# Optimization experiments

Hardware: AMD Instinct MI355X
Metric: run time of the kernel (lower is better)

The kernel has to match this reference:

```python
import jax, jax.numpy as jnp
import numpy as np


def setup_inputs() -> dict:
    key = jax.random.key(0)
    ks = jax.random.split(key, 12)
    C, H, L, P = 256, 8, 4, 4
    Lq, Lx = 2048, 300
    iss = jnp.array([[64, 64], [32, 32], [16, 16], [8, 8]], dtype=jnp.int32)
    Len_in = int(np.sum(np.array(iss)[:, 0] * np.array(iss)[:, 1]))  # 5440
    lsi = jnp.array([0, 4096, 5120, 5376], dtype=jnp.int32)
    return {
        "query": jax.random.normal(ks[0], (1, Lq, C), jnp.float32),
        "reference_points": jax.random.uniform(ks[1], (1, Lq, L, 2), jnp.float32),
        "input_flatten": jax.random.normal(ks[2], (1, Len_in, C), jnp.float32),
        "input_spatial_shapes": iss,
        "add_keys": jax.random.normal(ks[3], (1, Lx, C), jnp.float32),
        "input_level_start_index": lsi,
        "W_off": jax.random.normal(ks[4], (H * L * P * 2, C), jnp.float32) * 0.01,
        "b_off": jax.random.normal(ks[5], (H * L * P * 2,), jnp.float32),
        "W_attn": jax.random.normal(ks[6], (H * (L + 1), C, C), jnp.float32) * 0.05,
        "W_v": jax.random.normal(ks[7], (H * 2, C, C), jnp.float32) * 0.05,
        "b_v": jax.random.normal(ks[8], (H * 2, C), jnp.float32) * 0.01,
        "W_mix": jax.random.normal(ks[9], (C, H + 1), jnp.float32) * 0.5,
    }


def reference(query, reference_points, input_flatten, input_spatial_shapes,
              add_keys, input_level_start_index, W_off, b_off, W_attn, W_v, b_v, W_mix):
    N, Lq, C = query.shape
    L = input_spatial_shapes.shape[0]
    H = W_v.shape[0] // 2
    P = W_off.shape[0] // (H * L * 2)

    # sampling locations: ref (x,y in [0,1]) + offsets / (W,H)
    off = (query @ W_off.T + b_off).reshape(N, Lq, H, L, P, 2)
    wh = input_spatial_shapes[:, ::-1].astype(query.dtype)  # (L,2) = (W,H)
    loc = reference_points[:, :, None, :, None, :] + off / wh[None, None, None, :, None, :]

    # get_keys: truncating index computation + gather (faithful to original)
    loc = jnp.clip(loc, 0.0, 0.999)
    iss_f = input_spatial_shapes.astype(loc.dtype)[None, None, None, :, None, :]
    idx = (loc * iss_f).astype(jnp.int32)  # (N,Lq,H,L,P,2): (int(x*H_l), int(y*W_l))
    lin = (idx[..., 0]
           + idx[..., 1] * input_spatial_shapes[:, 0].astype(jnp.int32)[None, None, None, :, None]
           + input_level_start_index.astype(jnp.int32)[None, None, None, :, None])
    keys = input_flatten[0][lin[0]]                # (Lq,H,L,P,C)
    keys = jnp.transpose(keys, (1, 2, 3, 0, 4))    # (H,L,P,Lq,C)

    head_w = jax.nn.softmax(W_mix.T, axis=0)       # (H+1,C)
    qf = query[0]                                  # (Lq,C)
    ak = add_keys[0]                               # (Lx,C)

    # per-head, per-level similarity (replicates original overlapping index h*L+lvl)
    Ws = W_attn[jnp.arange(H)[:, None] * L + jnp.arange(L)[None, :]]  # (H,L,C,C)
    T = jnp.einsum('hlce,hlpqe->hlcpq', Ws, keys)  # (H,L,C,P,Lq)
    # faithful reshape quirk: (C, P*Lq) viewed as (P, Lq, C)
    T = T.reshape(H, L, P, Lq, C)
    attn_s = jnp.einsum('hlpqc,qc->hlpq', T, qf).reshape(H, L * P, Lq)

    Wadd = W_attn[jnp.arange(H) * L + L]           # (H,C,C)
    attn_a = jnp.einsum('xe,hce,qc->hxq', ak, Wadd, qf)  # (H,Lx,Lq)

    attn = jax.nn.softmax(jnp.concatenate([attn_s, attn_a], axis=1), axis=1)
    attn_s_sm, attn_a_sm = attn[:, :L * P], attn[:, L * P:]

    Wv0, bv0 = W_v[0::2], b_v[0::2]
    Wv1, bv1 = W_v[1::2], b_v[1::2]
    vals = (jnp.einsum('hlpqe,hce->hlpqc', keys, Wv0)
            + bv0[:, None, None, None, :]).reshape(H, L * P, Lq, C)
    v2 = jnp.einsum('xe,hce->hxc', ak, Wv1) + bv1[:, None, :]  # (H,Lx,C)

    out_h = (jnp.einsum('hkq,hkqc->hqc', attn_s_sm, vals)
             + jnp.einsum('hxq,hxc->hqc', attn_a_sm, v2))      # (H,Lq,C)
    result = qf * head_w[-1][None, :] + jnp.einsum('hqc,hc->qc', out_h, head_w[:-1])
    return result[None]
```

## Files before the change

kernel.cpp:

```cpp
#include <hip/hip_runtime.h>
#include <stdint.h>

#define NJ 316

typedef __attribute__((ext_vector_type(8))) short short8;
typedef __attribute__((ext_vector_type(4))) float f32x4;
union U4S8 { uint4 u; short8 s; };

__device__ __forceinline__ unsigned short f2bf(float x) {
    unsigned int u = __float_as_uint(x);
    u += 0x7fff + ((u >> 16) & 1);
    return (unsigned short)(u >> 16);
}
__device__ __forceinline__ float bf2f(unsigned short h) {
    return __uint_as_float(((unsigned int)h) << 16);
}

__global__ __launch_bounds__(256) void cvt_all_kernel(
    const float* __restrict__ q,  unsigned short* __restrict__ qh,  unsigned short* __restrict__ ql,
    const float* __restrict__ ak, unsigned short* __restrict__ akh, unsigned short* __restrict__ akl,
    const float* __restrict__ wv, unsigned short* __restrict__ wvh, unsigned short* __restrict__ wvl,
    const float* __restrict__ inflat, unsigned int* __restrict__ inflatP,
    const float* __restrict__ Wattn, unsigned short* __restrict__ wah, unsigned short* __restrict__ wal,
    unsigned short* __restrict__ v2th, unsigned short* __restrict__ v2tl)
{
    int i = blockIdx.x * 256 + threadIdx.x;
    if (i < 760576) {
        const float* s; unsigned short *dh, *dl; int off; bool pack = false;
        unsigned int* dp = nullptr;
        if (i < 131072)      { s = q;  dh = qh;  dl = ql;  off = i; }
        else if (i < 150272) { s = ak; dh = akh; dl = akl; off = i - 131072; }
        else if (i < 412416) { s = wv; dh = wvh; dl = wvl; off = i - 150272; }
        else { s = inflat; dp = inflatP; off = i - 412416; pack = true; dh = dl = nullptr; }
        float4 v = ((const float4*)s)[off];
        float x[4] = {v.x, v.y, v.z, v.w};
        unsigned short h[4], l[4];
        #pragma unroll
        for (int j = 0; j < 4; ++j) {
            h[j] = f2bf(x[j]);
            l[j] = f2bf(x[j] - bf2f(h[j]));
        }
        if (pack) {
            ((uint4*)dp)[off] = make_uint4(
                (unsigned)h[0] | ((unsigned)l[0] << 16),
                (unsigned)h[1] | ((unsigned)l[1] << 16),
                (unsigned)h[2] | ((unsigned)l[2] << 16),
                (unsigned)h[3] | ((unsigned)l[3] << 16));
        } else {
            ((uint2*)dh)[off] = make_uint2((unsigned)h[0] | ((unsigned)h[1] << 16),
                                           (unsigned)h[2] | ((unsigned)h[3] << 16));
            ((uint2*)dl)[off] = make_uint2((unsigned)l[0] | ((unsigned)l[1] << 16),
                                           (unsigned)l[2] | ((unsigned)l[3] << 16));
        }
    } else if (i < 891648) {
        int off = i - 760576;
        int base = off * 4;
        int z = base >> 16, r = base & 65535;
        float4 v = *(const float4*)&Wattn[(size_t)(4 * z + 4) * 65536 + r];
        float x[4] = {v.x, v.y, v.z, v.w};
        unsigned short h[4], l[4];
        #pragma unroll
        for (int j = 0; j < 4; ++j) {
            h[j] = f2bf(x[j]);
            l[j] = f2bf(x[j] - bf2f(h[j]));
        }
        ((uint2*)wah)[off] = make_uint2((unsigned)h[0] | ((unsigned)h[1] << 16),
                                        (unsigned)h[2] | ((unsigned)h[3] << 16));
        ((uint2*)wal)[off] = make_uint2((unsigned)l[0] | ((unsigned)l[1] << 16),
                                        (unsigned)l[2] | ((unsigned)l[3] << 16));
    } else {
        int j = i - 891648;
        size_t base = (size_t)j * 320;
        uint2 zz = make_uint2(0u, 0u);
        #pragma unroll
        for (int d = 0; d < 4; ++d) {
            ((uint2*)(v2th + base))[d] = zz;
            ((uint2*)(v2tl + base))[d] = zz;
        }
        ((uint2*)(v2th + base + 316))[0] = zz;
        ((uint2*)(v2tl + base + 316))[0] = zz;
    }
}

__global__ __launch_bounds__(256) void lin_kernel(
    const float* __restrict__ query, const float* __restrict__ refp,
    const int* __restrict__ iss, const int* __restrict__ lsi,
    const float* __restrict__ Woff, const float* __restrict__ boff,
    int* __restrict__ lin)
{
    __shared__ float qf8[8][256];
    __shared__ float wtile[256][33];
    __shared__ double offl[8][256];
    const int t = threadIdx.x;
    const int qbase = blockIdx.x * 8;
    #pragma unroll
    for (int i = 0; i < 8; ++i) qf8[i][t] = query[(qbase + i) * 256 + t];
    double acc[8];
    #pragma unroll
    for (int r = 0; r < 8; ++r) acc[r] = 0.0;
    for (int cb = 0; cb < 256; cb += 32) {
        __syncthreads();
        #pragma unroll
        for (int i = 0; i < 32; ++i) {
            int f = i * 256 + t;
            int o = f >> 5, jj = f & 31;
            wtile[o][jj] = Woff[o * 256 + cb + jj];
        }
        __syncthreads();
        #pragma unroll
        for (int jj = 0; jj < 32; ++jj) {
            double wv = (double)wtile[t][jj];
            #pragma unroll
            for (int r = 0; r < 8; ++r)
                acc[r] += (double)qf8[r][cb + jj] * wv;
        }
    }
    double bo = (double)boff[t];
    __syncthreads();
    #pragma unroll
    for (int r = 0; r < 8; ++r) offl[r][t] = acc[r] + bo;
    __syncthreads();
    #pragma unroll
    for (int rep = 0; rep < 4; ++rep) {
        int idx = rep * 256 + t;
        int r = idx >> 7;
        int s = idx & 127;
        int l = (s >> 2) & 3;
        int q = qbase + r;
        double offx = offl[r][2 * s];
        double offy = offl[r][2 * s + 1];
        int w0 = iss[l * 2 + 0];
        int w1 = iss[l * 2 + 1];
        double locx = (double)refp[q * 8 + l * 2 + 0] + offx / (double)w1;
        double locy = (double)refp[q * 8 + l * 2 + 1] + offy / (double)w0;
        locx = fmin(fmax(locx, 0.0), 0.999);
        locy = fmin(fmax(locy, 0.0), 0.999);
        int ix = (int)(locx * (double)w0);
        int iy = (int)(locy * (double)w1);
        lin[q * 128 + s] = ix + iy * w0 + lsi[l];
    }
}

__global__ __launch_bounds__(256, 3) void gattn_mfma(
    const unsigned short* __restrict__ qh, const unsigned short* __restrict__ ql,
    const unsigned int* __restrict__ inflatP, const float* __restrict__ Wattn,
    const int* __restrict__ lin, float* __restrict__ attn)
{
    __shared__ int linrow[256];
    __shared__ float Glds[16][268];
    const int t = threadIdx.x;
    const int lane = t & 63, w = t >> 6;
    const int b = blockIdx.x;
    const int qb = b & 7, p = (b >> 3) & 3, l = (b >> 5) & 3, h = b >> 7;
    linrow[t] = lin[(256 * qb + t) * 128 + h * 16 + l * 4 + p];
    __syncthreads();

    const int l15 = lane & 15, g = lane >> 4;
    const int q2l = qb + 8 * p + 32 * l15;
    const int ebase = 64 * w + l15;

    f32x4 acc[4][4];
    #pragma unroll
    for (int i = 0; i < 4; ++i)
        #pragma unroll
        for (int eg = 0; eg < 4; ++eg) acc[i][eg] = (f32x4){0.f, 0.f, 0.f, 0.f};

    for (int kb = 0; kb < 256; kb += 32) {
        U4S8 ah[4], al[4];
        #pragma unroll
        for (int i = 0; i < 4; ++i) {
            size_t off = (size_t)(q2l + 512 * i) * 256 + kb + 8 * g;
            ah[i].u = *(const uint4*)(qh + off);
            al[i].u = *(const uint4*)(ql + off);
        }
        int rowoff[8];
        #pragma unroll
        for (int m = 0; m < 8; ++m) rowoff[m] = linrow[kb + 8 * g + m] * 256;
        unsigned int uv[4][8];
        #pragma unroll
        for (int eg = 0; eg < 4; ++eg)
            #pragma unroll
            for (int m = 0; m < 8; ++m)
                uv[eg][m] = inflatP[rowoff[m] + ebase + 16 * eg];

        #pragma unroll
        for (int eg = 0; eg < 4; ++eg) {
            U4S8 bh, bl;
            unsigned int hh[4], ll[4];
            #pragma unroll
            for (int d = 0; d < 4; ++d) {
                hh[d] = __builtin_amdgcn_perm(uv[eg][2 * d + 1], uv[eg][2 * d],
                                              0x05040100u);
                ll[d] = __builtin_amdgcn_perm(uv[eg][2 * d + 1], uv[eg][2 * d],
                                              0x07060302u);
            }
            bh.u = make_uint4(hh[0], hh[1], hh[2], hh[3]);
            bl.u = make_uint4(ll[0], ll[1], ll[2], ll[3]);
            #pragma unroll
            for (int i = 0; i < 4; ++i) {
                acc[i][eg] = __builtin_amdgcn_mfma_f32_16x16x32_bf16(
                    ah[i].s, bh.s, acc[i][eg], 0, 0, 0);
                acc[i][eg] = __builtin_amdgcn_mfma_f32_16x16x32_bf16(
                    ah[i].s, bl.s, acc[i][eg], 0, 0, 0);
                acc[i][eg] = __builtin_amdgcn_mfma_f32_16x16x32_bf16(
                    al[i].s, bh.s, acc[i][eg], 0, 0, 0);
            }
        }
    }

    const int tx = t & 15, ty = t >> 4;
    const float* Wsbase = Wattn + (size_t)(h * 4 + l) * 65536;
    #pragma unroll
    for (int ci = 0; ci < 4; ++ci) {
        __syncthreads();
        #pragma unroll
        for (int eg = 0; eg < 4; ++eg)
            #pragma unroll
            for (int r = 0; r < 4; ++r)
                Glds[4 * g + r][64 * w + 16 * eg + l15] = acc[ci][eg][r];
        __syncthreads();
        const int hi = 16 * ci + ty;
        const int q2 = qb + 8 * p + 32 * hi;
        float gv[16];
        #pragma unroll
        for (int i2 = 0; i2 < 4; ++i2) {
            float4 gd = *(const float4*)&Glds[ty][tx * 4 + 64 * i2];
            gv[i2 * 4 + 0] = gd.x;
            gv[i2 * 4 + 1] = gd.y;
            gv[i2 * 4 + 2] = gd.z;
            gv[i2 * 4 + 3] = gd.w;
        }
        #pragma unroll
        for (int p2 = 0; p2 < 4; ++p2) {
            const float* wr = Wsbase + (size_t)(hi + 64 * p2) * 256;
            float partial = 0.f;
            #pragma unroll
            for (int i2 = 0; i2 < 4; ++i2) {
                float4 wv = *(const float4*)&wr[tx * 4 + 64 * i2];
                partial += wv.x * gv[i2 * 4 + 0] + wv.y * gv[i2 * 4 + 1]
                         + wv.z * gv[i2 * 4 + 2] + wv.w * gv[i2 * 4 + 3];
            }
            partial += __shfl_xor(partial, 1);
            partial += __shfl_xor(partial, 2);
            partial += __shfl_xor(partial, 4);
            partial += __shfl_xor(partial, 8);
            if (tx == 0)
                attn[((size_t)h * 2048 + q2) * NJ + (l * 4 + p2)] = partial;
        }
    }
}

struct Seg {
    const unsigned short *Ah, *Al, *Bh, *Bl;
    int K, lda, ldb;
    long sA, sB;
    int nprod;
};

template<bool ACCUM, bool OUTF32, int NSEG>
__global__ __launch_bounds__(256) void mfma_gemm(
    Seg s0, Seg s1,
    float* __restrict__ Cf, unsigned short* __restrict__ Ch,
    unsigned short* __restrict__ Cl,
    int M, int N, int ldc, long sC)
{
    __shared__ unsigned short As[2][64 * 40];
    __shared__ unsigned short Bs[2][128 * 40];
    const int t = threadIdx.x;
    const int lane = t & 63;
    const int wave = t >> 6;
    const int wm = (wave & 1) * 32, wn = (wave >> 1) * 64;
    const int nb = blockIdx.x * 128, mb = blockIdx.y * 64;
    const int z = blockIdx.z;

    f32x4 acc[2][4];
    #pragma unroll
    for (int i = 0; i < 2; ++i)
        #pragma unroll
        for (int j = 0; j < 4; ++j) acc[i][j] = (f32x4){0.f, 0.f, 0.f, 0.f};

    const int arow = t >> 2, akoff = (t & 3) * 8;
    const int frow = lane & 15, fk = (lane >> 4) * 8;

    #pragma unroll
    for (int seg = 0; seg < NSEG; ++seg) {
        const Seg S = seg ? s1 : s0;
        const int np = S.nprod;
        const unsigned short* Azh = S.Ah + (size_t)z * S.sA;
        const unsigned short* Azl = (np >= 2) ? S.Al + (size_t)z * S.sA : nullptr;
        const unsigned short* Bzh = S.Bh + (size_t)z * S.sB;
        const unsigned short* Bzl = (np >= 3) ? S.Bl + (size_t)z * S.sB : nullptr;
        for (int kb = 0; kb < S.K; kb += 32) {
            __syncthreads();
            {
                int gm = mb + arow;
                uint4 vh = {0, 0, 0, 0}, vl = {0, 0, 0, 0};
                if (gm < M) {
                    size_t o = (size_t)gm * S.lda + kb + akoff;
                    vh = *(const uint4*)(Azh + o);
                    if (np >= 2) vl = *(const uint4*)(Azl + o);
                }
                *(uint4*)&As[0][arow * 40 + akoff] = vh;
                if (np >= 2) *(uint4*)&As[1][arow * 40 + akoff] = vl;
                #pragma unroll
                for (int i = 0; i < 2; ++i) {
                    int f = i * 256 + t;
                    int brow = f >> 2, bkoff = (f & 3) * 8;
                    int gn = nb + brow;
                    uint4 wh = {0, 0, 0, 0}, wl = {0, 0, 0, 0};
                    if (gn < N) {
                        size_t o = (size_t)gn * S.ldb + kb + bkoff;
                        wh = *(const uint4*)(Bzh + o);
                        if (np >= 3) wl = *(const uint4*)(Bzl + o);
                    }
                    *(uint4*)&Bs[0][brow * 40 + bkoff] = wh;
                    if (np >= 3) *(uint4*)&Bs[1][brow * 40 + bkoff] = wl;
                }
            }
            __syncthreads();
            short8 a[2][2], b[4][2];
            #pragma unroll
            for (int i = 0; i < 2; ++i) {
                int r = wm + i * 16 + frow;
                a[i][0] = *(const short8*)&As[0][r * 40 + fk];
                if (np >= 2) a[i][1] = *(const short8*)&As[1][r * 40 + fk];
            }
            #pragma unroll
            for (int j = 0; j < 4; ++j) {
                int r = wn + j * 16 + frow;
                b[j][0] = *(const short8*)&Bs[0][r * 40 + fk];
                if (np >= 3) b[j][1] = *(const short8*)&Bs[1][r * 40 + fk];
            }
            #pragma unroll
            for (int i = 0; i < 2; ++i)
                #pragma unroll
                for (int j = 0; j < 4; ++j) {
                    acc[i][j] = __builtin_amdgcn_mfma_f32_16x16x32_bf16(
                        a[i][0], b[j][0], acc[i][j], 0, 0, 0);
                    if (np >= 2)
                        acc[i][j] = __builtin_amdgcn_mfma_f32_16x16x32_bf16(
                            a[i][1], b[j][0], acc[i][j], 0, 0, 0);
                    if (np >= 3)
                        acc[i][j] = __builtin_amdgcn_mfma_f32_16x16x32_bf16(
                            a[i][0], b[j][1], acc[i][j], 0, 0, 0);
                }
        }
    }
    #pragma unroll
    for (int i = 0; i < 2; ++i)
        #pragma unroll
        for (int r = 0; r < 4; ++r) {
            int gm = mb + wm + i * 16 + (lane >> 4) * 4 + r;
            if (gm >= M) continue;
            #pragma unroll
            for (int j = 0; j < 4; ++j) {
                int gn = nb + wn + j * 16 + (lane & 15);
                if (gn >= N) continue;
                size_t idx = (size_t)z * sC + (size_t)gm * ldc + gn;
                float v = acc[i][j][r];
                if (OUTF32) {
                    float prev = ACCUM ? Cf[idx] : 0.f;
                    Cf[idx] = prev + v;
                } else {
                    unsigned short h = f2bf(v);
                    Ch[idx] = h;
                    Cl[idx] = f2bf(v - bf2f(h));
                }
            }
        }
}

__global__ __launch_bounds__(256) void softmax_ka_kernel(
    const float* __restrict__ attn, const unsigned int* __restrict__ inflatP,
    const int* __restrict__ lin, float* __restrict__ s0,
    unsigned short* __restrict__ awh,
    unsigned short* __restrict__ KAh, unsigned short* __restrict__ KAl)
{
    __shared__ float red[8];
    __shared__ float w16[16];
    __shared__ int lls[16];
    const int t = threadIdx.x;
    const int lane = t & 63, w = t >> 6;
    const int rid = blockIdx.x;
    const int h = rid >> 11, q = rid & 2047;
    const float* row = attn + (size_t)rid * NJ;

    float v0 = row[t];
    float v1 = (t < 60) ? row[256 + t] : -1e30f;
    float m = fmaxf(v0, v1);
    #pragma unroll
    for (int d = 1; d < 64; d <<= 1) m = fmaxf(m, __shfl_xor(m, d));
    if (lane == 0) red[w] = m;
    __syncthreads();
    m = fmaxf(fmaxf(red[0], red[1]), fmaxf(red[2], red[3]));

    float e0 = expf(v0 - m);
    float e1 = (t < 60) ? expf(v1 - m) : 0.f;
    float s = e0 + e1;
    #pragma unroll
    for (int d = 1; d < 64; d <<= 1) s += __shfl_xor(s, d);
    if (lane == 0) red[4 + w] = s;
    __syncthreads();
    s = (red[4] + red[5]) + (red[6] + red[7]);
    const float inv = 1.f / s;

    float sf = (t < 16) ? e0 : 0.f;
    #pragma unroll
    for (int d = 1; d < 64; d <<= 1) sf += __shfl_xor(sf, d);
    if (lane == 0) red[w] = sf;

    float a0 = e0 * inv;
    float a1 = (t < 60) ? e1 * inv : 0.f;
    awh[(size_t)rid * 320 + t] = f2bf(a0);
    if (t < 64)
        awh[(size_t)rid * 320 + 256 + t] = f2bf(a1);
    if (t < 16) {
        w16[t] = a0;
        lls[t] = lin[q * 128 + h * 16 + t];
    }
    __syncthreads();
    if (t == 0)
        s0[rid] = ((red[0] + red[1]) + (red[2] + red[3])) * inv;

    float acc = 0.f;
    #pragma unroll
    for (int k = 0; k < 16; ++k) {
        unsigned int u = inflatP[lls[k] * 256 + t];
        acc += w16[k] * (bf2f((unsigned short)(u & 0xffff)) +
                         bf2f((unsigned short)(u >> 16)));
    }
    unsigned short hh = f2bf(acc);
    KAh[(size_t)rid * 256 + t] = hh;
    KAl[(size_t)rid * 256 + t] = f2bf(acc - bf2f(hh));
}

__global__ __launch_bounds__(256) void final_kernel(
    const float* __restrict__ qf, const float* __restrict__ OH,
    const float* __restrict__ s0, const float* __restrict__ bv,
    const float* __restrict__ Wmix, float* __restrict__ out)
{
    const int q = blockIdx.x, c = threadIdx.x;
    float wj[9], m = -1e30f;
    #pragma unroll
    for (int j = 0; j < 9; ++j) { wj[j] = Wmix[c * 9 + j]; m = fmaxf(m, wj[j]); }
    float s = 0.f;
    #pragma unroll
    for (int j = 0; j < 9; ++j) { wj[j] = expf(wj[j] - m); s += wj[j]; }
    float inv = 1.f / s;
    float acc = qf[q * 256 + c] * wj[8] * inv;
    #pragma unroll
    for (int h = 0; h < 8; ++h) {
        float s0v = s0[h * 2048 + q];
        float oh = OH[((size_t)h * 2048 + q) * 256 + c]
                 + s0v * bv[(2 * h) * 256 + c]
                 + (1.f - s0v) * bv[(2 * h + 1) * 256 + c];
        acc += oh * wj[h] * inv;
    }
    out[q * 256 + c] = acc;
}

extern "C" void kernel_launch(void* const* d_in, const int* in_sizes, int n_in,
                              void* d_out, int out_size, void* d_ws, size_t ws_size,
                              hipStream_t stream) {
    const float* query = (const float*)d_in[0];
    const float* refp  = (const float*)d_in[1];
    const float* inflat= (const float*)d_in[2];
    const int*   iss   = (const int*)d_in[3];
    const float* ak    = (const float*)d_in[4];
    const int*   lsi   = (const int*)d_in[5];
    const float* Woff  = (const float*)d_in[6];
    const float* boff  = (const float*)d_in[7];
    const float* Wattn = (const float*)d_in[8];
    const float* Wv    = (const float*)d_in[9];
    const float* bv    = (const float*)d_in[10];
    const float* Wmix  = (const float*)d_in[11];
    float* out = (float*)d_out;

    typedef unsigned short us;
    char* ws = (char*)d_ws;
    int* lin    = (int*)ws;   ws += (size_t)262144 * 4;
    float* attn = (float*)ws; ws += (size_t)8 * 2048 * NJ * 4;
    float* s0   = (float*)ws; ws += (size_t)8 * 2048 * 4;
    unsigned int* inflatP = (unsigned int*)ws; ws += (size_t)1392640 * 4;
    us* qh  = (us*)ws; ws += (size_t)524288 * 2;
    us* ql  = (us*)ws; ws += (size_t)524288 * 2;
    us* akh = (us*)ws; ws += (size_t)320 * 256 * 2;
    us* akl = (us*)ws; ws += (size_t)320 * 256 * 2;
    us* Waddh = (us*)ws; ws += (size_t)524288 * 2;
    us* Waddl = (us*)ws; ws += (size_t)524288 * 2;
    us* Wvh = (us*)ws; ws += (size_t)1048576 * 2;
    us* Wvl = (us*)ws; ws += (size_t)1048576 * 2;
    us* Bhh = (us*)ws; ws += (size_t)8 * 320 * 256 * 2;
    us* Bhl = (us*)ws; ws += (size_t)8 * 320 * 256 * 2;
    us* V2Th= (us*)ws; ws += (size_t)8 * 256 * 320 * 2;
    us* V2Tl= (us*)ws; ws += (size_t)8 * 256 * 320 * 2;
    us* awh = (us*)ws; ws += (size_t)8 * 2048 * 320 * 2;
    us* KAh = (us*)ws; ws += (size_t)8 * 2048 * 256 * 2;
    us* KAl = (us*)ws; ws += (size_t)8 * 2048 * 256 * 2;
    float* OH = (float*)ws;   ws += (size_t)8 * 2048 * 256 * 4;

    cvt_all_kernel<<<3491, 256, 0, stream>>>(
        query, qh, ql, ak, akh, akl, Wv, Wvh, Wvl,
        inflat, inflatP, Wattn, Waddh, Waddl, V2Th, V2Tl);
    lin_kernel<<<256, 256, 0, stream>>>(query, refp, iss, lsi, Woff, boff, lin);

    Seg sz = {nullptr, nullptr, nullptr, nullptr, 0, 0, 0, 0L, 0L, 0};

    {
        Seg a = {akh, akl, Waddh, Waddl, 256, 256, 256, 0L, 65536L, 3};
        mfma_gemm<false, false, 1><<<dim3(2, 5, 8), 256, 0, stream>>>(
            a, sz, nullptr, Bhh, Bhl, 300, 256, 256, 320L * 256);
    }
    {
        Seg a = {Wvh + 65536, Wvl + 65536, akh, nullptr, 256, 256, 256,
                 131072L, 0L, 2};
        mfma_gemm<false, false, 1><<<dim3(3, 4, 8), 256, 0, stream>>>(
            a, sz, nullptr, V2Th + 16, V2Tl + 16, 256, 300, 320, 256L * 320);
    }
    {
        Seg a = {qh, ql, Bhh, Bhl, 256, 256, 256, 0L, 320L * 256, 3};
        mfma_gemm<false, true, 1><<<dim3(3, 32, 8), 256, 0, stream>>>(
            a, sz, attn + 16, nullptr, nullptr, 2048, 300, NJ, 2048L * NJ);
    }

    gattn_mfma<<<1024, 256, 0, stream>>>(qh, ql, inflatP, Wattn, lin, attn);

    softmax_ka_kernel<<<16384, 256, 0, stream>>>(attn, inflatP, lin, s0,
                                                 awh, KAh, KAl);

    {
        Seg a = {KAh, KAl, Wvh, nullptr, 256, 256, 256, 2048L * 256,
                 2L * 65536, 2};
        Seg b = {awh, nullptr, V2Th, nullptr, 320, 320, 320, 2048L * 320,
                 256L * 320, 1};
        mfma_gemm<false, true, 2><<<dim3(2, 32, 8), 256, 0, stream>>>(
            a, b, OH, nullptr, nullptr, 2048, 256, 256, 2048L * 256);
    }

    final_kernel<<<2048, 256, 0, stream>>>(query, OH, s0, bv, Wmix, out);
}
```

Before: 296.1 us.

## Stage full gattn accumulator tile in LDS once; merge two small GEMMs into one launch

The gattn_mfma epilogue now writes all four 16-row accumulator chunks into a larger LDS buffer with a single barrier, instead of looping four times with two barriers each. The larger LDS footprint means occupancy is lowered from 3 to 2 blocks per CU. Separately, the two small add_keys GEMMs (Bh and V2T) are fused into one dual-dispatch kernel, saving a launch and letting both run concurrently. The risks are lower occupancy in gattn and higher register pressure from holding gv[4][16].

Measured after the change: 268.7 us, median of 2. 1.1x faster.

```diff
diff --git a/kernel.cpp b/kernel.cpp
--- a/kernel.cpp
+++ b/kernel.cpp
@@ -141,13 +141,13 @@
     }
 }
 
-__global__ __launch_bounds__(256, 3) void gattn_mfma(
+__global__ __launch_bounds__(256, 2) void gattn_mfma(
     const unsigned short* __restrict__ qh, const unsigned short* __restrict__ ql,
     const unsigned int* __restrict__ inflatP, const float* __restrict__ Wattn,
     const int* __restrict__ lin, float* __restrict__ attn)
 {
     __shared__ int linrow[256];
-    __shared__ float Glds[16][268];
+    __shared__ float Glds[64][268];
     const int t = threadIdx.x;
     const int lane = t & 63, w = t >> 6;
     const int b = blockIdx.x;
@@ -208,28 +208,32 @@
         }
     }
 
+    #pragma unroll
+    for (int i = 0; i < 4; ++i)
+        #pragma unroll
+        for (int eg = 0; eg < 4; ++eg)
+            #pragma unroll
+            for (int r = 0; r < 4; ++r)
+                Glds[16 * i + 4 * g + r][64 * w + 16 * eg + l15] = acc[i][eg][r];
+    __syncthreads();
+
     const int tx = t & 15, ty = t >> 4;
     const float* Wsbase = Wattn + (size_t)(h * 4 + l) * 65536;
-    #pragma unroll
-    for (int ci = 0; ci < 4; ++ci) {
-        __syncthreads();
-        #pragma unroll
-        for (int eg = 0; eg < 4; ++eg)
-            #pragma unroll
-            for (int r = 0; r < 4; ++r)
-                Glds[4 * g + r][64 * w + 16 * eg + l15] = acc[ci][eg][r];
-        __syncthreads();
-        const int hi = 16 * ci + ty;
-        const int q2 = qb + 8 * p + 32 * hi;
-        float gv[16];
+    float gv[4][16];
+    #pragma unroll
+    for (int r = 0; r < 4; ++r)
         #pragma unroll
         for (int i2 = 0; i2 < 4; ++i2) {
-            float4 gd = *(const float4*)&Glds[ty][tx * 4 + 64 * i2];
-            gv[i2 * 4 + 0] = gd.x;
-            gv[i2 * 4 + 1] = gd.y;
-            gv[i2 * 4 + 2] = gd.z;
-            gv[i2 * 4 + 3] = gd.w;
-        }
+            float4 gd = *(const float4*)&Glds[ty * 4 + r][tx * 4 + 64 * i2];
+            gv[r][i2 * 4 + 0] = gd.x;
+            gv[r][i2 * 4 + 1] = gd.y;
+            gv[r][i2 * 4 + 2] = gd.z;
+            gv[r][i2 * 4 + 3] = gd.w;
+        }
+    #pragma unroll
+    for (int r = 0; r < 4; ++r) {
+        int hi = ty * 4 + r;
+        int q2 = qb + 8 * p + 32 * hi;
         #pragma unroll
         for (int p2 = 0; p2 < 4; ++p2) {
             const float* wr = Wsbase + (size_t)(hi + 64 * p2) * 256;
@@ -237,8 +241,8 @@
             #pragma unroll
             for (int i2 = 0; i2 < 4; ++i2) {
                 float4 wv = *(const float4*)&wr[tx * 4 + 64 * i2];
-                partial += wv.x * gv[i2 * 4 + 0] + wv.y * gv[i2 * 4 + 1]
-                         + wv.z * gv[i2 * 4 + 2] + wv.w * gv[i2 * 4 + 3];
+                partial += wv.x * gv[r][i2 * 4 + 0] + wv.y * gv[r][i2 * 4 + 1]
+                         + wv.z * gv[r][i2 * 4 + 2] + wv.w * gv[r][i2 * 4 + 3];
             }
             partial += __shfl_xor(partial, 1);
             partial += __shfl_xor(partial, 2);
@@ -258,11 +262,11 @@
 };
 
 template<bool ACCUM, bool OUTF32, int NSEG>
-__global__ __launch_bounds__(256) void mfma_gemm(
-    Seg s0, Seg s1,
+__device__ __forceinline__ void gemm_core(
+    const Seg& s0, const Seg& s1,
     float* __restrict__ Cf, unsigned short* __restrict__ Ch,
     unsigned short* __restrict__ Cl,
-    int M, int N, int ldc, long sC)
+    int M, int N, int ldc, long sC, int nb, int mb, int z)
 {
     __shared__ unsigned short As[2][64 * 40];
     __shared__ unsigned short Bs[2][128 * 40];
@@ -270,8 +274,6 @@
     const int lane = t & 63;
     const int wave = t >> 6;
     const int wm = (wave & 1) * 32, wn = (wave >> 1) * 64;
-    const int nb = blockIdx.x * 128, mb = blockIdx.y * 64;
-    const int z = blockIdx.z;
 
     f32x4 acc[2][4];
     #pragma unroll
@@ -370,6 +372,41 @@
         }
 }
 
+template<bool ACCUM, bool OUTF32, int NSEG>
+__global__ __launch_bounds__(256) void mfma_gemm(
+    Seg s0, Seg s1,
+    float* __restrict__ Cf, unsigned short* __restrict__ Ch,
+    unsigned short* __restrict__ Cl,
+    int M, int N, int ldc, long sC)
+{
+    gemm_core<ACCUM, OUTF32, NSEG>(s0, s1, Cf, Ch, Cl, M, N, ldc, sC,
+                                   blockIdx.x * 128, blockIdx.y * 64,
+                                   blockIdx.z);
+}
+
+__global__ __launch_bounds__(256) void mfma_gemm_dual(
+    Seg a, int Ma, int Na, int ldca, long sCa,
+    unsigned short* __restrict__ Cha, unsigned short* __restrict__ Cla,
+    Seg b, int Mb, int Nb, int ldcb, long sCb,
+    unsigned short* __restrict__ Chb, unsigned short* __restrict__ Clb,
+    int ax)
+{
+    Seg dummy = a;
+    if ((int)blockIdx.x < ax) {
+        if ((int)blockIdx.y * 64 >= Ma) return;
+        gemm_core<false, false, 1>(a, dummy, nullptr, Cha, Cla,
+                                   Ma, Na, ldca, sCa,
+                                   blockIdx.x * 128, blockIdx.y * 64,
+                                   blockIdx.z);
+    } else {
+        if ((int)blockIdx.y * 64 >= Mb) return;
+        gemm_core<false, false, 1>(b, dummy, nullptr, Chb, Clb,
+                                   Mb, Nb, ldcb, sCb,
+                                   (blockIdx.x - ax) * 128, blockIdx.y * 64,
+                                   blockIdx.z);
+    }
+}
+
 __global__ __launch_bounds__(256) void softmax_ka_kernel(
     const float* __restrict__ attn, const unsigned int* __restrict__ inflatP,
     const int* __restrict__ lin, float* __restrict__ s0,
@@ -508,14 +545,11 @@
 
     {
         Seg a = {akh, akl, Waddh, Waddl, 256, 256, 256, 0L, 65536L, 3};
-        mfma_gemm<false, false, 1><<<dim3(2, 5, 8), 256, 0, stream>>>(
-            a, sz, nullptr, Bhh, Bhl, 300, 256, 256, 320L * 256);
-    }
-    {
-        Seg a = {Wvh + 65536, Wvl + 65536, akh, nullptr, 256, 256, 256,
+        Seg b = {Wvh + 65536, Wvl + 65536, akh, nullptr, 256, 256, 256,
                  131072L, 0L, 2};
-        mfma_gemm<false, false, 1><<<dim3(3, 4, 8), 256, 0, stream>>>(
-            a, sz, nullptr, V2Th + 16, V2Tl + 16, 256, 300, 320, 256L * 320);
+        mfma_gemm_dual<<<dim3(5, 5, 8), 256, 0, stream>>>(
+            a, 300, 256, 256, 320L * 256, Bhh, Bhl,
+            b, 256, 300, 320, 256L * 320, V2Th + 16, V2Tl + 16, 2);
     }
     {
         Seg a = {qh, ql, Bhh, Bhl, 256, 256, 256, 0L, 320L * 256, 3};
```
